# Optimization experiments

Hardware: AMD Instinct MI355X
Metric: run time of the kernel (lower is better)

## Reference

```python
import jax, jax.numpy as jnp
import numpy as np

N_NODES = 200000
N_EDGES = 6400000
F_IN = 128
HID = 128
N_GRAPHS = 64


def setup_inputs() -> dict:
    key = jax.random.key(0)
    ks = jax.random.split(key, 10)
    x = jax.random.normal(ks[0], (N_NODES, F_IN), dtype=jnp.float32)
    edge_index = jax.random.randint(ks[1], (2, N_EDGES), 0, N_NODES, dtype=jnp.int32)
    edge_weight = jax.random.uniform(ks[2], (N_EDGES,), dtype=jnp.float32)
    batch = jnp.sort(jax.random.randint(ks[3], (N_NODES,), 0, N_GRAPHS, dtype=jnp.int32))
    s1 = 1.0 / np.sqrt(F_IN)
    s2 = 1.0 / np.sqrt(HID)
    W1 = jax.random.normal(ks[4], (F_IN, HID), dtype=jnp.float32) * s1
    b1 = jnp.zeros((HID,), dtype=jnp.float32)
    W2 = jax.random.normal(ks[5], (HID, HID), dtype=jnp.float32) * s2
    b2 = jnp.zeros((HID,), dtype=jnp.float32)
    Wfc = jax.random.normal(ks[6], (HID, 1), dtype=jnp.float32) * s2
    bfc = jnp.zeros((1,), dtype=jnp.float32)
    return {"x": x, "edge_index": edge_index, "edge_weight": edge_weight,
            "batch": batch, "W1": W1, "b1": b1, "W2": W2, "b2": b2,
            "Wfc": Wfc, "bfc": bfc}


def gcn_conv(x, src, dst, ew, W, b):
    # PyG GCNConv: add self-loops (weight 1), symmetric normalization,
    # linear transform, scatter-add aggregation at destination, plus bias.
    n = x.shape[0]
    loop = jnp.arange(n, dtype=src.dtype)
    src_f = jnp.concatenate([src, loop])
    dst_f = jnp.concatenate([dst, loop])
    ew_f = jnp.concatenate([ew, jnp.ones((n,), dtype=ew.dtype)])
    deg = jax.ops.segment_sum(ew_f, dst_f, num_segments=n)
    dinv = jnp.where(deg > 0, jax.lax.rsqrt(deg), 0.0)
    norm = dinv[src_f] * ew_f * dinv[dst_f]  # [E+n]
    h = x @ W  # [n, H]
    out = jax.ops.segment_sum(norm[:, None] * h[src_f], dst_f, num_segments=n)
    return out + b


def reference(x, edge_index, edge_weight, batch, W1, b1, W2, b2, Wfc, bfc):
    src, dst = edge_index[0], edge_index[1]
    h = gcn_conv(x, src, dst, edge_weight, W1, b1)
    h = jax.nn.elu(h)  # ELU applied after all but the last conv layer
    h = gcn_conv(h, src, dst, edge_weight, W2, b2)
    # global mean pool over graphs
    counts = jax.ops.segment_sum(jnp.ones((h.shape[0],), h.dtype), batch,
                                 num_segments=N_GRAPHS)
    sums = jax.ops.segment_sum(h, batch, num_segments=N_GRAPHS)
    pooled = sums / jnp.maximum(counts, 1.0)[:, None]
    return pooled @ Wfc + bfc
```

## Files before the change

### kernel.cpp

```cpp
#include <hip/hip_runtime.h>
#include <hip/hip_bf16.h>


#define NODES_PER_BLOCK 4

__global__ void init_kernel(float* __restrict__ deg, int* __restrict__ cnt,
                            float* __restrict__ gsum, int* __restrict__ gcnt, int n) {
    int i = blockIdx.x * blockDim.x + threadIdx.x;
    if (i < n) { deg[i] = 1.0f; cnt[i] = 0; }
    if (i < 64) { gsum[i] = 0.0f; gcnt[i] = 0; }
}

__global__ void edge_pass1(const int* __restrict__ dst, const float* __restrict__ ew,
                           float* __restrict__ deg, int* __restrict__ cnt, int E) {
    int e = blockIdx.x * blockDim.x + threadIdx.x;
    if (e >= E) return;
    int d = dst[e];
    atomicAdd(&deg[d], ew[e]);
    atomicAdd(&cnt[d], 1);
}

__global__ void compute_dinv(float* __restrict__ deg, int n) {
    int i = blockIdx.x * blockDim.x + threadIdx.x;
    if (i < n) deg[i] = rsqrtf(deg[i]);
}

__global__ void scan_block(const int* __restrict__ cnt, int* __restrict__ rowptr,
                           int* __restrict__ partial, int n) {
    __shared__ int lds[256];
    int t = threadIdx.x;
    int i = blockIdx.x * 256 + t;
    int v = (i < n) ? cnt[i] : 0;
    lds[t] = v;
    __syncthreads();
    for (int off = 1; off < 256; off <<= 1) {
        int add = (t >= off) ? lds[t - off] : 0;
        __syncthreads();
        lds[t] += add;
        __syncthreads();
    }
    if (i < n) rowptr[i] = lds[t] - v;
    if (t == 255) partial[blockIdx.x] = lds[255];
}

__global__ void scan_partial(int* __restrict__ partial, int nb) {
    __shared__ int lds[1024];
    int t = threadIdx.x;
    int v = (t < nb) ? partial[t] : 0;
    lds[t] = v;
    __syncthreads();
    for (int off = 1; off < 1024; off <<= 1) {
        int add = (t >= off) ? lds[t - off] : 0;
        __syncthreads();
        lds[t] += add;
        __syncthreads();
    }
    if (t < nb) partial[t] = lds[t] - v;
}

__global__ void finalize_rowptr(int* __restrict__ rowptr, const int* __restrict__ partial,
                                int* __restrict__ cursor, int n, int e_total) {
    int i = blockIdx.x * 256 + threadIdx.x;
    if (i < n) {
        int v = rowptr[i] + partial[blockIdx.x];
        rowptr[i] = v;
        cursor[i] = v;
    }
    if (i == 0) rowptr[n] = e_total;
}

__global__ void edge_fill(const int* __restrict__ src, const int* __restrict__ dst,
                          const float* __restrict__ ew, const float* __restrict__ dinv,
                          int* __restrict__ cursor, int2* __restrict__ edges, int E) {
    int e = blockIdx.x * blockDim.x + threadIdx.x;
    if (e >= E) return;
    int s = src[e], d = dst[e];
    float w = dinv[s] * ew[e] * dinv[d];
    int pos = atomicAdd(&cursor[d], 1);
    edges[pos] = make_int2(s, __float_as_int(w));
}

__global__ __launch_bounds__(256, 2) void matmul_fc(const float* __restrict__ X,
                                                    const float* __restrict__ W,
                                                    float* __restrict__ Y, int n) {
    int wib = threadIdx.x >> 6, lane = threadIdx.x & 63;
    int wid = blockIdx.x * 4 + wib;
    int half = wid & 1;
    int col = (half << 6) | lane;
    float Wreg[128];
#pragma unroll
    for (int k = 0; k < 128; k++) Wreg[k] = W[k * 128 + col];
    int stride = (gridDim.x * 4) >> 1;
    for (int nn = wid >> 1; nn < n; nn += stride) {
        const float4* xr = (const float4*)(X + (size_t)nn * 128);
        float a0 = 0.f, a1 = 0.f;
#pragma unroll
        for (int k4 = 0; k4 < 32; k4 += 2) {
            float4 xa = xr[k4];
            float4 xb = xr[k4 + 1];
            a0 = fmaf(xa.x, Wreg[4 * k4 + 0], a0);
            a0 = fmaf(xa.y, Wreg[4 * k4 + 1], a0);
            a0 = fmaf(xa.z, Wreg[4 * k4 + 2], a0);
            a0 = fmaf(xa.w, Wreg[4 * k4 + 3], a0);
            a1 = fmaf(xb.x, Wreg[4 * k4 + 4], a1);
            a1 = fmaf(xb.y, Wreg[4 * k4 + 5], a1);
            a1 = fmaf(xb.z, Wreg[4 * k4 + 6], a1);
            a1 = fmaf(xb.w, Wreg[4 * k4 + 7], a1);
        }
        Y[(size_t)nn * 128 + col] = a0 + a1;
    }
}

__device__ __forceinline__ float2 gather_row(const float2* __restrict__ Hf2,
                                             const int2* __restrict__ edges,
                                             int beg, int end, int lane, float2 init) {
    float2 a0 = init;
    float2 a1 = make_float2(0.f, 0.f);
    float2 a2 = make_float2(0.f, 0.f);
    float2 a3 = make_float2(0.f, 0.f);
    for (int base = beg; base < end; base += 64) {
        int cnt = end - base; if (cnt > 64) cnt = 64;
        int2 ed = make_int2(0, 0);
        if (lane < cnt) ed = edges[base + lane];
        int es = ed.x;
        float ef = __int_as_float(ed.y);
        int cnt8 = (cnt + 7) & ~7;
        for (int j = 0; j < cnt8; j += 8) {
            int s0 = __shfl(es, j + 0), s1 = __shfl(es, j + 1);
            int s2 = __shfl(es, j + 2), s3 = __shfl(es, j + 3);
            int s4 = __shfl(es, j + 4), s5 = __shfl(es, j + 5);
            int s6 = __shfl(es, j + 6), s7 = __shfl(es, j + 7);
            float w0 = __shfl(ef, j + 0), w1 = __shfl(ef, j + 1);
            float w2 = __shfl(ef, j + 2), w3 = __shfl(ef, j + 3);
            float w4 = __shfl(ef, j + 4), w5 = __shfl(ef, j + 5);
            float w6 = __shfl(ef, j + 6), w7 = __shfl(ef, j + 7);
            float2 h0 = Hf2[(size_t)s0 * 64 + lane];
            float2 h1 = Hf2[(size_t)s1 * 64 + lane];
            float2 h2 = Hf2[(size_t)s2 * 64 + lane];
            float2 h3 = Hf2[(size_t)s3 * 64 + lane];
            float2 h4 = Hf2[(size_t)s4 * 64 + lane];
            float2 h5 = Hf2[(size_t)s5 * 64 + lane];
            float2 h6 = Hf2[(size_t)s6 * 64 + lane];
            float2 h7 = Hf2[(size_t)s7 * 64 + lane];
            a0.x = fmaf(w0, h0.x, a0.x); a0.y = fmaf(w0, h0.y, a0.y);
            a1.x = fmaf(w1, h1.x, a1.x); a1.y = fmaf(w1, h1.y, a1.y);
            a2.x = fmaf(w2, h2.x, a2.x); a2.y = fmaf(w2, h2.y, a2.y);
            a3.x = fmaf(w3, h3.x, a3.x); a3.y = fmaf(w3, h3.y, a3.y);
            a0.x = fmaf(w4, h4.x, a0.x); a0.y = fmaf(w4, h4.y, a0.y);
            a1.x = fmaf(w5, h5.x, a1.x); a1.y = fmaf(w5, h5.y, a1.y);
            a2.x = fmaf(w6, h6.x, a2.x); a2.y = fmaf(w6, h6.y, a2.y);
            a3.x = fmaf(w7, h7.x, a3.x); a3.y = fmaf(w7, h7.y, a3.y);
        }
    }
    a0.x += a1.x + a2.x + a3.x;
    a0.y += a1.y + a2.y + a3.y;
    return a0;
}

__global__ __launch_bounds__(256) void agg_elu(const float* __restrict__ H,
                                               const int2* __restrict__ edges,
                                               const int* __restrict__ rowptr,
                                               const float* __restrict__ dinv,
                                               const float* __restrict__ bias,
                                               float* __restrict__ out, int n) {
    int w = threadIdx.x >> 6, lane = threadIdx.x & 63;
    int node = blockIdx.x * NODES_PER_BLOCK + w;
    if (node >= n) return;
    const float2* Hf2 = (const float2*)H;
    float di = dinv[node];
    float sw = di * di;
    float2 own = Hf2[(size_t)node * 64 + lane];
    float2 acc = gather_row(Hf2, edges, rowptr[node], rowptr[node + 1], lane,
                            make_float2(own.x * sw, own.y * sw));
    float ox = acc.x + bias[2 * lane];
    float oy = acc.y + bias[2 * lane + 1];
    ox = ox > 0.f ? ox : expm1f(ox);
    oy = oy > 0.f ? oy : expm1f(oy);
    ((float2*)out)[(size_t)node * 64 + lane] = make_float2(ox, oy);
}

__global__ __launch_bounds__(256) void agg_pool(const float* __restrict__ H,
                                                const int2* __restrict__ edges,
                                                const int* __restrict__ rowptr,
                                                const float* __restrict__ dinv,
                                                const float* __restrict__ bias,
                                                const float* __restrict__ wfc,
                                                const int* __restrict__ batch,
                                                float* __restrict__ gsum,
                                                int* __restrict__ gcnt, int n) {
    int w = threadIdx.x >> 6, lane = threadIdx.x & 63;
    int node = blockIdx.x * NODES_PER_BLOCK + w;
    if (node >= n) return;
    const float2* Hf2 = (const float2*)H;
    float di = dinv[node];
    float sw = di * di;
    float2 own = Hf2[(size_t)node * 64 + lane];
    float2 acc = gather_row(Hf2, edges, rowptr[node], rowptr[node + 1], lane,
                            make_float2(own.x * sw, own.y * sw));
    float px = acc.x + bias[2 * lane];
    float py = acc.y + bias[2 * lane + 1];
    float partial = px * wfc[2 * lane] + py * wfc[2 * lane + 1];
#pragma unroll
    for (int off = 32; off; off >>= 1) partial += __shfl_xor(partial, off);
    if (lane == 0) {
        int g = batch[node];
        atomicAdd(&gsum[g], partial);
        atomicAdd(&gcnt[g], 1);
    }
}

__global__ void finalize_out(const float* __restrict__ gsum, const int* __restrict__ gcnt,
                             const float* __restrict__ bfc, float* __restrict__ out) {
    int g = threadIdx.x;
    if (g < 64) {
        float c = (float)gcnt[g];
        out[g] = gsum[g] / fmaxf(c, 1.0f) + bfc[0];
    }
}

extern "C" void kernel_launch(void* const* d_in, const int* in_sizes, int n_in,
                              void* d_out, int out_size, void* d_ws, size_t ws_size,
                              hipStream_t stream) {
    const int N = in_sizes[0] / 128;
    const int E = in_sizes[2];

    const float* x     = (const float*)d_in[0];
    const int*   ei    = (const int*)d_in[1];
    const int*   src   = ei;
    const int*   dst   = ei + E;
    const float* ew    = (const float*)d_in[2];
    const int*   batch = (const int*)d_in[3];
    const float* W1    = (const float*)d_in[4];
    const float* b1    = (const float*)d_in[5];
    const float* W2    = (const float*)d_in[6];
    const float* b2    = (const float*)d_in[7];
    const float* Wfc   = (const float*)d_in[8];
    const float* bfc   = (const float*)d_in[9];
    float* out = (float*)d_out;

    char* base = (char*)d_ws;
    size_t off = 0;
    auto carve = [&](size_t bytes) -> void* {
        void* r = base + off;
        off = (off + bytes + 255) & ~(size_t)255;
        return r;
    };
    float* hA      = (float*)carve((size_t)N * 128 * 4);
    float* hB      = (float*)carve((size_t)N * 128 * 4);
    int2*  edges   = (int2*) carve((size_t)E * 8);
    float* deg     = (float*)carve((size_t)N * 4);
    int*   rowptr  = (int*)  carve((size_t)(N + 1) * 4);
    int*   cursor  = (int*)  carve((size_t)N * 4);
    int*   partial = (int*)  carve(1024 * 4);
    float* gsum    = (float*)carve(64 * 4);
    int*   gcnt    = (int*)  carve(64 * 4);

    const int NB = (N + 255) / 256;
    const int EB = (E + 255) / 256;
    const int AGGB = (N + NODES_PER_BLOCK - 1) / NODES_PER_BLOCK;

    hipLaunchKernelGGL(init_kernel, dim3(NB), dim3(256), 0, stream, deg, cursor, gsum, gcnt, N);
    hipLaunchKernelGGL(edge_pass1, dim3(EB), dim3(256), 0, stream, dst, ew, deg, cursor, E);
    hipLaunchKernelGGL(compute_dinv, dim3(NB), dim3(256), 0, stream, deg, N);
    hipLaunchKernelGGL(scan_block, dim3(NB), dim3(256), 0, stream, cursor, rowptr, partial, N);
    hipLaunchKernelGGL(scan_partial, dim3(1), dim3(1024), 0, stream, partial, NB);
    hipLaunchKernelGGL(finalize_rowptr, dim3(NB), dim3(256), 0, stream, rowptr, partial, cursor, N, E);
    hipLaunchKernelGGL(edge_fill, dim3(EB), dim3(256), 0, stream, src, dst, ew, deg, cursor, edges, E);
    hipLaunchKernelGGL(matmul_fc, dim3(2048), dim3(256), 0, stream, x, W1, hA, N);
    hipLaunchKernelGGL(agg_elu, dim3(AGGB), dim3(256), 0, stream, hA, edges, rowptr, deg, b1, hB, N);
    hipLaunchKernelGGL(matmul_fc, dim3(2048), dim3(256), 0, stream, hB, W2, hA, N);
    hipLaunchKernelGGL(agg_pool, dim3(AGGB), dim3(256), 0, stream, hA, edges, rowptr, deg, b2, Wfc, batch, gsum, gcnt, N);
    hipLaunchKernelGGL(finalize_out, dim3(1), dim3(64), 0, stream, gsum, gcnt, bfc, out);
}
```

Measured before the change: 5.369 ms.

## Store hidden features in bf16 and pipeline gather loads with inline asm

Intermediate node feature matrices are now stored as bf16 instead of fp32, which halves the bytes moved by the random-access edge gather and by the matmul reads and writes. The gather loop is rewritten to issue 16 dword loads per batch in inline asm, double-buffered with explicit vmcnt waits so loads overlap the FMAs. Occupancy hints are raised on the aggregation kernels. The cost is reduced precision in the hidden activations, plus hand-written asm that bypasses compiler scheduling and could be fragile.

```diff
diff --git a/kernel.cpp b/kernel.cpp
--- a/kernel.cpp
+++ b/kernel.cpp
@@ -3,6 +3,13 @@
 
 
 #define NODES_PER_BLOCK 4
+
+__device__ __forceinline__ unsigned int f32_to_bf16(float f) {
+    unsigned int u = __float_as_uint(f);
+    return (u + 0x7FFFu + ((u >> 16) & 1u)) >> 16;
+}
+__device__ __forceinline__ float bf16lo(unsigned int u) { return __uint_as_float(u << 16); }
+__device__ __forceinline__ float bf16hi(unsigned int u) { return __uint_as_float(u & 0xFFFF0000u); }
 
 __global__ void init_kernel(float* __restrict__ deg, int* __restrict__ cnt,
                             float* __restrict__ gsum, int* __restrict__ gcnt, int n) {
@@ -80,9 +87,10 @@
     edges[pos] = make_int2(s, __float_as_int(w));
 }
 
-__global__ __launch_bounds__(256, 2) void matmul_fc(const float* __restrict__ X,
+template <bool BF16IN>
+__global__ __launch_bounds__(256, 2) void matmul_fc(const void* __restrict__ Xv,
                                                     const float* __restrict__ W,
-                                                    float* __restrict__ Y, int n) {
+                                                    unsigned short* __restrict__ Y, int n) {
     int wib = threadIdx.x >> 6, lane = threadIdx.x & 63;
     int wid = blockIdx.x * 4 + wib;
     int half = wid & 1;
@@ -92,111 +100,191 @@
     for (int k = 0; k < 128; k++) Wreg[k] = W[k * 128 + col];
     int stride = (gridDim.x * 4) >> 1;
     for (int nn = wid >> 1; nn < n; nn += stride) {
-        const float4* xr = (const float4*)(X + (size_t)nn * 128);
         float a0 = 0.f, a1 = 0.f;
+        if constexpr (BF16IN) {
+            const uint4* xr = (const uint4*)((const char*)Xv + (size_t)nn * 256);
 #pragma unroll
-        for (int k4 = 0; k4 < 32; k4 += 2) {
-            float4 xa = xr[k4];
-            float4 xb = xr[k4 + 1];
-            a0 = fmaf(xa.x, Wreg[4 * k4 + 0], a0);
-            a0 = fmaf(xa.y, Wreg[4 * k4 + 1], a0);
-            a0 = fmaf(xa.z, Wreg[4 * k4 + 2], a0);
-            a0 = fmaf(xa.w, Wreg[4 * k4 + 3], a0);
-            a1 = fmaf(xb.x, Wreg[4 * k4 + 4], a1);
-            a1 = fmaf(xb.y, Wreg[4 * k4 + 5], a1);
-            a1 = fmaf(xb.z, Wreg[4 * k4 + 6], a1);
-            a1 = fmaf(xb.w, Wreg[4 * k4 + 7], a1);
+            for (int q = 0; q < 16; ++q) {
+                uint4 u = xr[q];
+                int k = q * 8;
+                a0 = fmaf(bf16lo(u.x), Wreg[k + 0], a0); a1 = fmaf(bf16hi(u.x), Wreg[k + 1], a1);
+                a0 = fmaf(bf16lo(u.y), Wreg[k + 2], a0); a1 = fmaf(bf16hi(u.y), Wreg[k + 3], a1);
+                a0 = fmaf(bf16lo(u.z), Wreg[k + 4], a0); a1 = fmaf(bf16hi(u.z), Wreg[k + 5], a1);
+                a0 = fmaf(bf16lo(u.w), Wreg[k + 6], a0); a1 = fmaf(bf16hi(u.w), Wreg[k + 7], a1);
+            }
+        } else {
+            const float4* xr = (const float4*)((const float*)Xv + (size_t)nn * 128);
+#pragma unroll
+            for (int k4 = 0; k4 < 32; k4 += 2) {
+                float4 xa = xr[k4];
+                float4 xb = xr[k4 + 1];
+                a0 = fmaf(xa.x, Wreg[4 * k4 + 0], a0);
+                a0 = fmaf(xa.y, Wreg[4 * k4 + 1], a0);
+                a0 = fmaf(xa.z, Wreg[4 * k4 + 2], a0);
+                a0 = fmaf(xa.w, Wreg[4 * k4 + 3], a0);
+                a1 = fmaf(xb.x, Wreg[4 * k4 + 4], a1);
+                a1 = fmaf(xb.y, Wreg[4 * k4 + 5], a1);
+                a1 = fmaf(xb.z, Wreg[4 * k4 + 6], a1);
+                a1 = fmaf(xb.w, Wreg[4 * k4 + 7], a1);
+            }
         }
-        Y[(size_t)nn * 128 + col] = a0 + a1;
-    }
-}
-
-__device__ __forceinline__ float2 gather_row(const float2* __restrict__ Hf2,
-                                             const int2* __restrict__ edges,
-                                             int beg, int end, int lane, float2 init) {
+        Y[(size_t)nn * 128 + col] = (unsigned short)f32_to_bf16(a0 + a1);
+    }
+}
+
+__device__ __forceinline__ float2 gather_row_bf16(const unsigned short* __restrict__ H,
+                                                  const int2* __restrict__ edges,
+                                                  int beg, int end, int lane, float2 init) {
     float2 a0 = init;
     float2 a1 = make_float2(0.f, 0.f);
     float2 a2 = make_float2(0.f, 0.f);
     float2 a3 = make_float2(0.f, 0.f);
+    const int lane4 = lane << 2;
+    const unsigned long long hb = (unsigned long long)H;
     for (int base = beg; base < end; base += 64) {
         int cnt = end - base; if (cnt > 64) cnt = 64;
         int2 ed = make_int2(0, 0);
         if (lane < cnt) ed = edges[base + lane];
         int es = ed.x;
         float ef = __int_as_float(ed.y);
-        int cnt8 = (cnt + 7) & ~7;
-        for (int j = 0; j < cnt8; j += 8) {
-            int s0 = __shfl(es, j + 0), s1 = __shfl(es, j + 1);
-            int s2 = __shfl(es, j + 2), s3 = __shfl(es, j + 3);
-            int s4 = __shfl(es, j + 4), s5 = __shfl(es, j + 5);
-            int s6 = __shfl(es, j + 6), s7 = __shfl(es, j + 7);
-            float w0 = __shfl(ef, j + 0), w1 = __shfl(ef, j + 1);
-            float w2 = __shfl(ef, j + 2), w3 = __shfl(ef, j + 3);
-            float w4 = __shfl(ef, j + 4), w5 = __shfl(ef, j + 5);
-            float w6 = __shfl(ef, j + 6), w7 = __shfl(ef, j + 7);
-            float2 h0 = Hf2[(size_t)s0 * 64 + lane];
-            float2 h1 = Hf2[(size_t)s1 * 64 + lane];
-            float2 h2 = Hf2[(size_t)s2 * 64 + lane];
-            float2 h3 = Hf2[(size_t)s3 * 64 + lane];
-            float2 h4 = Hf2[(size_t)s4 * 64 + lane];
-            float2 h5 = Hf2[(size_t)s5 * 64 + lane];
-            float2 h6 = Hf2[(size_t)s6 * 64 + lane];
-            float2 h7 = Hf2[(size_t)s7 * 64 + lane];
-            a0.x = fmaf(w0, h0.x, a0.x); a0.y = fmaf(w0, h0.y, a0.y);
-            a1.x = fmaf(w1, h1.x, a1.x); a1.y = fmaf(w1, h1.y, a1.y);
-            a2.x = fmaf(w2, h2.x, a2.x); a2.y = fmaf(w2, h2.y, a2.y);
-            a3.x = fmaf(w3, h3.x, a3.x); a3.y = fmaf(w3, h3.y, a3.y);
-            a0.x = fmaf(w4, h4.x, a0.x); a0.y = fmaf(w4, h4.y, a0.y);
-            a1.x = fmaf(w5, h5.x, a1.x); a1.y = fmaf(w5, h5.y, a1.y);
-            a2.x = fmaf(w6, h6.x, a2.x); a2.y = fmaf(w6, h6.y, a2.y);
-            a3.x = fmaf(w7, h7.x, a3.x); a3.y = fmaf(w7, h7.y, a3.y);
+        int nb = (cnt + 15) >> 4;
+        unsigned int hA0,hA1,hA2_,hA3,hA4,hA5,hA6,hA7,hA8,hA9,hA10,hA11,hA12,hA13,hA14,hA15;
+        unsigned int hB0,hB1,hB2,hB3,hB4,hB5,hB6,hB7,hB8,hB9,hB10,hB11,hB12,hB13,hB14,hB15;
+        float wA0,wA1,wA2,wA3,wA4,wA5,wA6,wA7,wA8,wA9,wA10,wA11,wA12,wA13,wA14,wA15;
+        float wB0,wB1,wB2,wB3,wB4,wB5,wB6,wB7,wB8,wB9,wB10,wB11,wB12,wB13,wB14,wB15;
+        int o0,o1,o2,o3,o4,o5,o6,o7,o8,o9,o10,o11,o12,o13,o14,o15;
+
+#define GRAB16(L, j) \
+    o0=(__shfl(es,(j)+0)<<8)|lane4;  w##L##0=__shfl(ef,(j)+0); \
+    o1=(__shfl(es,(j)+1)<<8)|lane4;  w##L##1=__shfl(ef,(j)+1); \
+    o2=(__shfl(es,(j)+2)<<8)|lane4;  w##L##2=__shfl(ef,(j)+2); \
+    o3=(__shfl(es,(j)+3)<<8)|lane4;  w##L##3=__shfl(ef,(j)+3); \
+    o4=(__shfl(es,(j)+4)<<8)|lane4;  w##L##4=__shfl(ef,(j)+4); \
+    o5=(__shfl(es,(j)+5)<<8)|lane4;  w##L##5=__shfl(ef,(j)+5); \
+    o6=(__shfl(es,(j)+6)<<8)|lane4;  w##L##6=__shfl(ef,(j)+6); \
+    o7=(__shfl(es,(j)+7)<<8)|lane4;  w##L##7=__shfl(ef,(j)+7); \
+    o8=(__shfl(es,(j)+8)<<8)|lane4;  w##L##8=__shfl(ef,(j)+8); \
+    o9=(__shfl(es,(j)+9)<<8)|lane4;  w##L##9=__shfl(ef,(j)+9); \
+    o10=(__shfl(es,(j)+10)<<8)|lane4; w##L##10=__shfl(ef,(j)+10); \
+    o11=(__shfl(es,(j)+11)<<8)|lane4; w##L##11=__shfl(ef,(j)+11); \
+    o12=(__shfl(es,(j)+12)<<8)|lane4; w##L##12=__shfl(ef,(j)+12); \
+    o13=(__shfl(es,(j)+13)<<8)|lane4; w##L##13=__shfl(ef,(j)+13); \
+    o14=(__shfl(es,(j)+14)<<8)|lane4; w##L##14=__shfl(ef,(j)+14); \
+    o15=(__shfl(es,(j)+15)<<8)|lane4; w##L##15=__shfl(ef,(j)+15);
+
+#define ISSUE8(d0,d1,d2,d3,d4,d5,d6,d7, s0,s1,s2,s3,s4,s5,s6,s7) \
+    asm volatile( \
+        "global_load_dword %0, %8,  %16\n\t" \
+        "global_load_dword %1, %9,  %16\n\t" \
+        "global_load_dword %2, %10, %16\n\t" \
+        "global_load_dword %3, %11, %16\n\t" \
+        "global_load_dword %4, %12, %16\n\t" \
+        "global_load_dword %5, %13, %16\n\t" \
+        "global_load_dword %6, %14, %16\n\t" \
+        "global_load_dword %7, %15, %16" \
+        : "=&v"(d0), "=&v"(d1), "=&v"(d2), "=&v"(d3), \
+          "=&v"(d4), "=&v"(d5), "=&v"(d6), "=&v"(d7) \
+        : "v"(s0), "v"(s1), "v"(s2), "v"(s3), \
+          "v"(s4), "v"(s5), "v"(s6), "v"(s7), "s"(hb));
+
+#define ISSUE_A ISSUE8(hA0,hA1,hA2_,hA3,hA4,hA5,hA6,hA7, o0,o1,o2,o3,o4,o5,o6,o7) \
+                ISSUE8(hA8,hA9,hA10,hA11,hA12,hA13,hA14,hA15, o8,o9,o10,o11,o12,o13,o14,o15)
+#define ISSUE_B ISSUE8(hB0,hB1,hB2,hB3,hB4,hB5,hB6,hB7, o0,o1,o2,o3,o4,o5,o6,o7) \
+                ISSUE8(hB8,hB9,hB10,hB11,hB12,hB13,hB14,hB15, o8,o9,o10,o11,o12,o13,o14,o15)
+
+#define WAIT16 asm volatile("s_waitcnt vmcnt(16)" ::: "memory"); __builtin_amdgcn_sched_barrier(0);
+#define WAIT0  asm volatile("s_waitcnt vmcnt(0)"  ::: "memory"); __builtin_amdgcn_sched_barrier(0);
+
+#define ACC1(L, g, ac) ac.x = fmaf(w##L##g, bf16lo(h##L##g), ac.x); \
+                       ac.y = fmaf(w##L##g, bf16hi(h##L##g), ac.y);
+#define FMA_A ACC1(A,0,a0) ACC1(A,1,a1) ACC1(A,2_,a2) ACC1(A,3,a3) \
+              ACC1(A,4,a0) ACC1(A,5,a1) ACC1(A,6,a2)  ACC1(A,7,a3) \
+              ACC1(A,8,a0) ACC1(A,9,a1) ACC1(A,10,a2) ACC1(A,11,a3) \
+              ACC1(A,12,a0) ACC1(A,13,a1) ACC1(A,14,a2) ACC1(A,15,a3)
+#define FMA_B ACC1(B,0,a0) ACC1(B,1,a1) ACC1(B,2,a2)  ACC1(B,3,a3) \
+              ACC1(B,4,a0) ACC1(B,5,a1) ACC1(B,6,a2)  ACC1(B,7,a3) \
+              ACC1(B,8,a0) ACC1(B,9,a1) ACC1(B,10,a2) ACC1(B,11,a3) \
+              ACC1(B,12,a0) ACC1(B,13,a1) ACC1(B,14,a2) ACC1(B,15,a3)
+
+        float wA2_ = 0.f;
+        if (nb == 1) {
+            GRAB16(A, 0) wA2_ = wA2; ISSUE_A
+            WAIT0 FMA_A
+        } else if (nb == 2) {
+            GRAB16(A, 0) wA2_ = wA2; ISSUE_A
+            GRAB16(B, 16) ISSUE_B
+            WAIT16 FMA_A
+            WAIT0  FMA_B
+        } else if (nb == 3) {
+            GRAB16(A, 0) wA2_ = wA2; ISSUE_A
+            GRAB16(B, 16) ISSUE_B
+            WAIT16 FMA_A
+            GRAB16(A, 32) wA2_ = wA2; ISSUE_A
+            WAIT16 FMA_B
+            WAIT0  FMA_A
+        } else {
+            GRAB16(A, 0) wA2_ = wA2; ISSUE_A
+            GRAB16(B, 16) ISSUE_B
+            WAIT16 FMA_A
+            GRAB16(A, 32) wA2_ = wA2; ISSUE_A
+            WAIT16 FMA_B
+            GRAB16(B, 48) ISSUE_B
+            WAIT16 FMA_A
+            WAIT0  FMA_B
         }
+#undef GRAB16
+#undef ISSUE8
+#undef ISSUE_A
+#undef ISSUE_B
+#undef WAIT16
+#undef WAIT0
+#undef ACC1
+#undef FMA_A
+#undef FMA_B
     }
     a0.x += a1.x + a2.x + a3.x;
     a0.y += a1.y + a2.y + a3.y;
     return a0;
 }
 
-__global__ __launch_bounds__(256) void agg_elu(const float* __restrict__ H,
-                                               const int2* __restrict__ edges,
-                                               const int* __restrict__ rowptr,
-                                               const float* __restrict__ dinv,
-                                               const float* __restrict__ bias,
-                                               float* __restrict__ out, int n) {
+__global__ __launch_bounds__(256, 4) void agg_elu(const unsigned short* __restrict__ H,
+                                                  const int2* __restrict__ edges,
+                                                  const int* __restrict__ rowptr,
+                                                  const float* __restrict__ dinv,
+                                                  const float* __restrict__ bias,
+                                                  unsigned short* __restrict__ out, int n) {
     int w = threadIdx.x >> 6, lane = threadIdx.x & 63;
     int node = blockIdx.x * NODES_PER_BLOCK + w;
     if (node >= n) return;
-    const float2* Hf2 = (const float2*)H;
     float di = dinv[node];
     float sw = di * di;
-    float2 own = Hf2[(size_t)node * 64 + lane];
-    float2 acc = gather_row(Hf2, edges, rowptr[node], rowptr[node + 1], lane,
-                            make_float2(own.x * sw, own.y * sw));
+    unsigned int ow = ((const unsigned int*)H)[(size_t)node * 64 + lane];
+    float2 acc = gather_row_bf16(H, edges, rowptr[node], rowptr[node + 1], lane,
+                                 make_float2(bf16lo(ow) * sw, bf16hi(ow) * sw));
     float ox = acc.x + bias[2 * lane];
     float oy = acc.y + bias[2 * lane + 1];
     ox = ox > 0.f ? ox : expm1f(ox);
     oy = oy > 0.f ? oy : expm1f(oy);
-    ((float2*)out)[(size_t)node * 64 + lane] = make_float2(ox, oy);
-}
-
-__global__ __launch_bounds__(256) void agg_pool(const float* __restrict__ H,
-                                                const int2* __restrict__ edges,
-                                                const int* __restrict__ rowptr,
-                                                const float* __restrict__ dinv,
-                                                const float* __restrict__ bias,
-                                                const float* __restrict__ wfc,
-                                                const int* __restrict__ batch,
-                                                float* __restrict__ gsum,
-                                                int* __restrict__ gcnt, int n) {
+    ((unsigned int*)out)[(size_t)node * 64 + lane] = f32_to_bf16(ox) | (f32_to_bf16(oy) << 16);
+}
+
+__global__ __launch_bounds__(256, 4) void agg_pool(const unsigned short* __restrict__ H,
+                                                   const int2* __restrict__ edges,
+                                                   const int* __restrict__ rowptr,
+                                                   const float* __restrict__ dinv,
+                                                   const float* __restrict__ bias,
+                                                   const float* __restrict__ wfc,
+                                                   const int* __restrict__ batch,
+                                                   float* __restrict__ gsum,
+                                                   int* __restrict__ gcnt, int n) {
     int w = threadIdx.x >> 6, lane = threadIdx.x & 63;
     int node = blockIdx.x * NODES_PER_BLOCK + w;
     if (node >= n) return;
-    const float2* Hf2 = (const float2*)H;
     float di = dinv[node];
     float sw = di * di;
-    float2 own = Hf2[(size_t)node * 64 + lane];
-    float2 acc = gather_row(Hf2, edges, rowptr[node], rowptr[node + 1], lane,
-                            make_float2(own.x * sw, own.y * sw));
+    unsigned int ow = ((const unsigned int*)H)[(size_t)node * 64 + lane];
+    float2 acc = gather_row_bf16(H, edges, rowptr[node], rowptr[node + 1], lane,
+                                 make_float2(bf16lo(ow) * sw, bf16hi(ow) * sw));
     float px = acc.x + bias[2 * lane];
     float py = acc.y + bias[2 * lane + 1];
     float partial = px * wfc[2 * lane] + py * wfc[2 * lane + 1];
@@ -245,8 +333,8 @@
         off = (off + bytes + 255) & ~(size_t)255;
         return r;
     };
-    float* hA      = (float*)carve((size_t)N * 128 * 4);
-    float* hB      = (float*)carve((size_t)N * 128 * 4);
+    unsigned short* t1 = (unsigned short*)carve((size_t)N * 128 * 2);
+    unsigned short* t2 = (unsigned short*)carve((size_t)N * 128 * 2);
     int2*  edges   = (int2*) carve((size_t)E * 8);
     float* deg     = (float*)carve((size_t)N * 4);
     int*   rowptr  = (int*)  carve((size_t)(N + 1) * 4);
@@ -266,9 +354,9 @@
     hipLaunchKernelGGL(scan_partial, dim3(1), dim3(1024), 0, stream, partial, NB);
     hipLaunchKernelGGL(finalize_rowptr, dim3(NB), dim3(256), 0, stream, rowptr, partial, cursor, N, E);
     hipLaunchKernelGGL(edge_fill, dim3(EB), dim3(256), 0, stream, src, dst, ew, deg, cursor, edges, E);
-    hipLaunchKernelGGL(matmul_fc, dim3(2048), dim3(256), 0, stream, x, W1, hA, N);
-    hipLaunchKernelGGL(agg_elu, dim3(AGGB), dim3(256), 0, stream, hA, edges, rowptr, deg, b1, hB, N);
-    hipLaunchKernelGGL(matmul_fc, dim3(2048), dim3(256), 0, stream, hB, W2, hA, N);
-    hipLaunchKernelGGL(agg_pool, dim3(AGGB), dim3(256), 0, stream, hA, edges, rowptr, deg, b2, Wfc, batch, gsum, gcnt, N);
+    hipLaunchKernelGGL((matmul_fc<false>), dim3(2048), dim3(256), 0, stream, (const void*)x, W1, t1, N);
+    hipLaunchKernelGGL(agg_elu, dim3(AGGB), dim3(256), 0, stream, t1, edges, rowptr, deg, b1, t2, N);
+    hipLaunchKernelGGL((matmul_fc<true>), dim3(2048), dim3(256), 0, stream, (const void*)t2, W2, t1, N);
+    hipLaunchKernelGGL(agg_pool, dim3(AGGB), dim3(256), 0, stream, t1, edges, rowptr, deg, b2, Wfc, batch, gsum, gcnt, N);
     hipLaunchKernelGGL(finalize_out, dim3(1), dim3(64), 0, stream, gsum, gcnt, bfc, out);
 }
```

Result: slower. 5.813 ms (+8.3%).
